# Kernel optimization log

Measured on AMD Instinct MI355X. Metric: run time of the kernel, lower is better.

Reference implementation:

```python
import jax, jax.numpy as jnp
import numpy as np

N = 100000   # nodes
S = 2        # layout samples per graph
G = 8        # graphs in batch
E = 400000   # directed edges
MID = 256    # mid_ch
L = 4        # n_layer
CLN = 2      # concat_last_n
IN_CH = 53 + 32 + 6 * 23 + 6 * 3 + 6 * 4  # 265


def setup_inputs() -> dict:
    key = jax.random.key(0)
    ks = jax.random.split(key, 16)
    f = lambda k, sh: jax.random.normal(k, sh, dtype=jnp.float32)
    return {
        "x_feat": f(ks[0], (N, 53)),
        "dim_feat": f(ks[1], (N, 6, 23)),
        "layout_feat": f(ks[2], (N, S, 6, 4)),
        "tile_feat": f(ks[3], (G, S, 6, 3)),
        "opcode_embed": f(ks[4], (121, 32)) * 0.02,
        "preW": f(ks[5], (IN_CH, MID)) * 0.05,
        "preb": jnp.zeros((MID,), jnp.float32),
        "convWl": f(ks[6], (L, MID, MID // 2)) * 0.05,
        "convWr": f(ks[7], (L, MID, MID // 2)) * 0.05,
        "convb": jnp.zeros((L, MID // 2), jnp.float32),
        "revWl": f(ks[8], (L, MID, MID // 2)) * 0.05,
        "revWr": f(ks[9], (L, MID, MID // 2)) * 0.05,
        "revb": jnp.zeros((L, MID // 2), jnp.float32),
        "headW": f(ks[10], (MID * CLN, 1)) * 0.05,
        "headb": jnp.zeros((1,), jnp.float32),
        "node_opcode": jax.random.randint(ks[11], (N,), 0, 121),
        "batch": jnp.sort(jax.random.randint(ks[12], (N,), 0, G)),
        "edge_index": jax.random.randint(ks[13], (2, E), 0, N),
    }


def _sage(x, src, tgt, inv_deg, Wl, Wr, b):
    # PyG SAGEConv: out = lin_l(mean_{j->i} x_j) + lin_r(x_i) + bias
    # x: [S, N, C]; gather messages from src, scatter-add into tgt.
    agg = jnp.zeros_like(x).at[:, tgt].add(x[:, src])
    agg = agg * inv_deg[None, :, None]
    return (jnp.einsum('snc,co->sno', agg, Wl)
            + jnp.einsum('snc,co->sno', x, Wr) + b)


def reference(x_feat, dim_feat, layout_feat, tile_feat, opcode_embed,
              preW, preb, convWl, convWr, convb, revWl, revWr, revb,
              headW, headb, node_opcode, batch, edge_index):
    op = opcode_embed[node_opcode]                       # [N, 32]
    base = jnp.concatenate([x_feat, op, dim_feat.reshape(N, -1)], axis=-1)
    x = jnp.concatenate([
        jnp.broadcast_to(base[None], (S,) + base.shape),          # [S,N,223]
        layout_feat.transpose(1, 0, 2, 3).reshape(S, N, -1),       # [S,N,24]
        tile_feat[batch].transpose(1, 0, 2, 3).reshape(S, N, -1),  # [S,N,18]
    ], axis=-1)                                                    # [S,N,265]
    x = jax.nn.relu(x @ preW + preb)                               # [S,N,MID]

    src, tgt = edge_index[0], edge_index[1]
    one = jnp.ones((E,), x.dtype)
    inv_fwd = 1.0 / jnp.maximum(jnp.zeros((N,), x.dtype).at[tgt].add(one), 1.0)
    inv_rev = 1.0 / jnp.maximum(jnp.zeros((N,), x.dtype).at[src].add(one), 1.0)

    xs = []
    for i in range(L):
        x = jnp.concatenate([
            _sage(x, src, tgt, inv_fwd, convWl[i], convWr[i], convb[i]),
            _sage(x, tgt, src, inv_rev, revWl[i], revWr[i], revb[i]),
        ], axis=-1)
        x = jax.nn.relu(x)
        if i >= L - CLN:
            xs.append(x)
    x = jnp.concatenate(xs, axis=-1)                     # [S, N, MID*CLN]

    pooled = jnp.zeros((S, G, x.shape[-1]), x.dtype).at[:, batch].add(x)
    out = pooled @ headW + headb                         # [S, G, 1]
    return out.transpose(1, 0, 2)                        # [G, S, 1]
```

## Files before the change

kernel.cpp:

```cpp
#include <hip/hip_runtime.h>
#include <hip/hip_bf16.h>

#define N_NODES 100000
#define S_SAMP 2
#define G_GRAPH 8
#define E_EDGES 400000
#define NLAYER 4
#define IN_CH 265
#define KBASE 256
#define MT128 ((N_NODES + 127) / 128)
#define NPAD (MT128 * 128)
#define NG128 ((MT128 + 7) / 8)
#define NB1 ((N_NODES + 1023) / 1024)

typedef unsigned short u16;
typedef unsigned int u32;
typedef short bf16x8 __attribute__((ext_vector_type(8)));
typedef float f32x4 __attribute__((ext_vector_type(4)));

__device__ __forceinline__ float b2f(u16 u) {
    union { u32 i; float f; } x; x.i = ((u32)u) << 16; return x.f;
}
__device__ __forceinline__ u16 f2b(float f) {
    __hip_bfloat16 h = __float2bfloat16(f);
    return *reinterpret_cast<u16*>(&h);
}

__device__ __forceinline__ void gl_lds16(const u16* g, u16* l) {
    __builtin_amdgcn_global_load_lds(
        (const __attribute__((address_space(1))) void*)g,
        (__attribute__((address_space(3))) void*)l, 16, 0, 0);
}

__global__ __launch_bounds__(256) void build_base_k(const float* __restrict__ xf,
                                                    const float* __restrict__ dimf,
                                                    const float* __restrict__ opemb,
                                                    const int* __restrict__ opcode,
                                                    u16* __restrict__ xb) {
    int item = blockIdx.x * blockDim.x + threadIdx.x;
    int n = item >> 6;
    if (n >= N_NODES) return;
    int base = (item & 63) * 4;
    int opc = opcode[n];
    ushort4 o;
    u16* op = &o.x;
    #pragma unroll
    for (int u = 0; u < 4; u++) {
        int c = base + u;
        float v = 0.0f;
        if (c < 53)       v = xf[(size_t)n * 53 + c];
        else if (c < 85)  v = opemb[opc * 32 + (c - 53)];
        else if (c < 223) v = dimf[(size_t)n * 138 + (c - 85)];
        op[u] = f2b(v);
    }
    *(ushort4*)(xb + (size_t)n * KBASE + base) = o;
}

__global__ void pack_w_k(const float* __restrict__ cWl, const float* __restrict__ rWl,
                         const float* __restrict__ cWr, const float* __restrict__ rWr,
                         const float* __restrict__ cb,  const float* __restrict__ rb,
                         u16* __restrict__ Wt, float* __restrict__ bcat) {
    int idx = blockIdx.x * blockDim.x + threadIdx.x;
    if (idx < NLAYER * 512 * 256) {
        int l = idx >> 17;
        int r = idx & 131071;
        int j = r >> 8;
        int k = r & 255;
        int jj = j & 255;
        int half = j >> 8;
        int sub = jj >> 7;
        int col = jj & 127;
        const float* src = half ? (sub ? rWl : cWl) : (sub ? rWr : cWr);
        Wt[idx] = f2b(src[((size_t)l * 256 + k) * 128 + col]);
    }
    if (idx < NLAYER * 512) {
        int l = idx >> 9;
        int j = idx & 511;
        float v = 0.0f;
        if (j < 256) v = (j < 128) ? cb[l * 128 + j] : rb[l * 128 + (j - 128)];
        bcat[idx] = v;
    }
}

__global__ void pack_pre_k(const float* __restrict__ preW, u16* __restrict__ preWt) {
    int idx = blockIdx.x * blockDim.x + threadIdx.x;
    if (idx >= 256 * KBASE) return;
    int j = idx >> 8;
    int k = idx & 255;
    preWt[idx] = (k < 223) ? f2b(preW[(size_t)k * 256 + j]) : (u16)0;
}

__global__ void tvec_k(const float* __restrict__ tilef, const float* __restrict__ preW,
                       float* __restrict__ tvec) {
    int idx = blockIdx.x * blockDim.x + threadIdx.x;
    if (idx >= G_GRAPH * S_SAMP * 256) return;
    int c = idx & 255;
    int gs = idx >> 8;
    float a = 0.0f;
    #pragma unroll
    for (int k = 0; k < 18; k++)
        a += tilef[gs * 18 + k] * preW[(size_t)(247 + k) * 256 + c];
    tvec[idx] = a;
}

__global__ void deg_k(const int* __restrict__ ei, int* __restrict__ degF,
                      int* __restrict__ degR) {
    int e = blockIdx.x * blockDim.x + threadIdx.x;
    if (e < E_EDGES) {
        atomicAdd(&degF[ei[E_EDGES + e]], 1);
        atomicAdd(&degR[ei[e]], 1);
    }
}

__global__ __launch_bounds__(1024) void scan1_k(const int* __restrict__ degF,
                                                const int* __restrict__ degR,
                                                int* __restrict__ rpF,
                                                int* __restrict__ rpR,
                                                int* __restrict__ bsum) {
    const int* deg = blockIdx.y ? degR : degF;
    int* rp = blockIdx.y ? rpR : rpF;
    __shared__ int buf[1024];
    int i = blockIdx.x * 1024 + threadIdx.x;
    int v = (i < N_NODES) ? deg[i] : 0;
    buf[threadIdx.x] = v;
    __syncthreads();
    for (int off = 1; off < 1024; off <<= 1) {
        int t = (threadIdx.x >= off) ? buf[threadIdx.x - off] : 0;
        __syncthreads();
        buf[threadIdx.x] += t;
        __syncthreads();
    }
    if (i < N_NODES) rp[i] = buf[threadIdx.x] - v;
    if (threadIdx.x == 1023) bsum[blockIdx.y * NB1 + blockIdx.x] = buf[1023];
}

__global__ __launch_bounds__(256) void scan2_k(int* __restrict__ bsum,
                                               int* __restrict__ rpF,
                                               int* __restrict__ rpR) {
    __shared__ int buf[2][128];
    int half = threadIdx.x >> 7;
    int t = threadIdx.x & 127;
    int v = (t < NB1) ? bsum[half * NB1 + t] : 0;
    buf[half][t] = v;
    __syncthreads();
    for (int off = 1; off < 128; off <<= 1) {
        int x = (t >= off) ? buf[half][t - off] : 0;
        __syncthreads();
        buf[half][t] += x;
        __syncthreads();
    }
    if (t < NB1) bsum[half * NB1 + t] = buf[half][t] - v;
    if (t == NB1) (half ? rpR : rpF)[N_NODES] = buf[half][NB1 - 1];
}

__global__ void scan3_k(const int* __restrict__ bsum, int* __restrict__ rpF,
                        int* __restrict__ rpR) {
    int* rp = blockIdx.y ? rpR : rpF;
    int i = blockIdx.x * 1024 + threadIdx.x;
    if (i < N_NODES) rp[i] += bsum[blockIdx.y * NB1 + blockIdx.x];
}

__global__ void inv_cursor_k(const int* __restrict__ degF, const int* __restrict__ degR,
                             const int* __restrict__ rpF, const int* __restrict__ rpR,
                             float* __restrict__ invF, float* __restrict__ invR,
                             int* __restrict__ curF, int* __restrict__ curR) {
    int i = blockIdx.x * blockDim.x + threadIdx.x;
    if (i < N_NODES) {
        invF[i] = 1.0f / fmaxf((float)degF[i], 1.0f);
        invR[i] = 1.0f / fmaxf((float)degR[i], 1.0f);
        curF[i] = rpF[i];
        curR[i] = rpR[i];
    }
}

__global__ void fill_k(const int* __restrict__ ei, int* __restrict__ curF,
                       int* __restrict__ curR, int* __restrict__ colF,
                       int* __restrict__ colR) {
    int e = blockIdx.x * blockDim.x + threadIdx.x;
    if (e < E_EDGES) {
        int s = ei[e], t = ei[E_EDGES + e];
        colF[atomicAdd(&curF[t], 1)] = s;
        colR[atomicAdd(&curR[s], 1)] = t;
    }
}

template <bool RELU_OUT, int NCHUNK, int COLT>
__global__ __launch_bounds__(256) void mmB_k(const u16* __restrict__ A,
                                             const u16* __restrict__ Bt,
                                             const float* __restrict__ bias,
                                             u16* __restrict__ C0,
                                             u16* __restrict__ C1,
                                             int M) {
    __shared__ u16 As[128 * 128];
    __shared__ u16 Bs[64 * 128];
    constexpr int K = NCHUNK * 128;

    int bid = blockIdx.x;
    int x = bid & 7;
    int q = bid >> 3;
    int c = q % COLT;
    int g = q / COLT;
    int rowTile = g * 8 + x;
    if (rowTile >= MT128) return;
    int rowBase = rowTile * 128;
    int colBase = c * 64;

    int tid = threadIdx.x;
    int wv = tid >> 6;
    int lane = tid & 63;
    int quad = lane >> 4;
    int l16 = lane & 15;
    int rsub = lane >> 4;
    int sl = lane & 15;

    f32x4 acc[2][4] = {};

    for (int ci = 0; ci < NCHUNK; ci++) {
        int k0 = ci * 128;
        #pragma unroll
        for (int i = 0; i < 8; i++) {
            int r = wv * 32 + 4 * i + rsub;
            int ch = sl ^ (r & 15);
            gl_lds16(A + (size_t)(rowBase + r) * K + k0 + ch * 8,
                     As + (wv * 32 + 4 * i) * 128);
        }
        #pragma unroll
        for (int i = 0; i < 4; i++) {
            int r = wv * 16 + 4 * i + rsub;
            int ch = sl ^ (r & 15);
            gl_lds16(Bt + (size_t)(colBase + r) * K + k0 + ch * 8,
                     Bs + (wv * 16 + 4 * i) * 128);
        }
        __syncthreads();
        #pragma unroll
        for (int ks = 0; ks < 4; ks++) {
            int ca = ks * 4 + quad;
            bf16x8 af[2];
            #pragma unroll
            for (int rf = 0; rf < 2; rf++) {
                int ra = wv * 32 + rf * 16 + l16;
                af[rf] = *(const bf16x8*)(As + ra * 128 + (ca ^ (ra & 15)) * 8);
            }
            #pragma unroll
            for (int cf = 0; cf < 4; cf++) {
                int rb = cf * 16 + l16;
                bf16x8 bf = *(const bf16x8*)(Bs + rb * 128 + (ca ^ (rb & 15)) * 8);
                acc[0][cf] = __builtin_amdgcn_mfma_f32_16x16x32_bf16(af[0], bf, acc[0][cf], 0, 0, 0);
                acc[1][cf] = __builtin_amdgcn_mfma_f32_16x16x32_bf16(af[1], bf, acc[1][cf], 0, 0, 0);
            }
        }
        if (ci + 1 < NCHUNK) __syncthreads();
    }

    u16* dst = (colBase < 256) ? C0 : C1;
    int cb = colBase & 255;
    #pragma unroll
    for (int rf = 0; rf < 2; rf++) {
        #pragma unroll
        for (int cf = 0; cf < 4; cf++) {
            int col = cb + cf * 16 + l16;
            float bv = bias[colBase + cf * 16 + l16];
            #pragma unroll
            for (int r = 0; r < 4; r++) {
                int row = rowBase + wv * 32 + rf * 16 + quad * 4 + r;
                if (row < M) {
                    float v = acc[rf][cf][r] + bv;
                    if (RELU_OUT) v = fmaxf(v, 0.0f);
                    dst[(size_t)row * 256 + col] = f2b(v);
                }
            }
        }
    }
}

__global__ __launch_bounds__(256) void pre_fix_k(const u16* __restrict__ Xmid,
                                                 const float* __restrict__ layf,
                                                 const float* __restrict__ preW,
                                                 const float* __restrict__ tvec,
                                                 const int* __restrict__ batch,
                                                 int s, u16* __restrict__ X0) {
    __shared__ float tv[G_GRAPH * 256];
    for (int i = threadIdx.x; i < G_GRAPH * 256; i += 256) {
        int g = i >> 8, c = i & 255;
        tv[i] = tvec[(g * S_SAMP + s) * 256 + c];
    }
    __syncthreads();

    int wv = threadIdx.x >> 6;
    int lane = threadIdx.x & 63;
    int c0 = lane * 4;

    float4 W[24];
    #pragma unroll
    for (int k = 0; k < 24; k++)
        W[k] = *(const float4*)(preW + (size_t)(223 + k) * 256 + c0);

    for (int n = blockIdx.x * 4 + wv; n < N_NODES; n += gridDim.x * 4) {
        int g = batch[n];
        float4 L4[6];
        const float4* lp = (const float4*)(layf + ((size_t)n * S_SAMP + s) * 24);
        #pragma unroll
        for (int q = 0; q < 6; q++) L4[q] = lp[q];
        const float* l = (const float*)L4;
        float4 t4 = *(const float4*)&tv[g * 256 + c0];
        float a0 = t4.x, a1 = t4.y, a2 = t4.z, a3 = t4.w;
        #pragma unroll
        for (int k = 0; k < 24; k++) {
            float lk = l[k];
            a0 += lk * W[k].x;
            a1 += lk * W[k].y;
            a2 += lk * W[k].z;
            a3 += lk * W[k].w;
        }
        ushort4 m = *(const ushort4*)(Xmid + (size_t)n * 256 + c0);
        ushort4 o;
        o.x = f2b(fmaxf(b2f(m.x) + a0, 0.0f));
        o.y = f2b(fmaxf(b2f(m.y) + a1, 0.0f));
        o.z = f2b(fmaxf(b2f(m.z) + a2, 0.0f));
        o.w = f2b(fmaxf(b2f(m.w) + a3, 0.0f));
        *(ushort4*)(X0 + (size_t)n * 256 + c0) = o;
    }
}

template <bool DOT>
__global__ __launch_bounds__(256) void agg_k(const int* __restrict__ rpF,
                                             const int* __restrict__ colF,
                                             const int* __restrict__ rpR,
                                             const int* __restrict__ colR,
                                             const float* __restrict__ invF,
                                             const float* __restrict__ invR,
                                             const u16* __restrict__ H,
                                             u16* __restrict__ Xn,
                                             const float* __restrict__ w,
                                             float* __restrict__ dotbuf) {
    int n = (blockIdx.x * blockDim.x + threadIdx.x) >> 6;
    if (n >= N_NODES) return;
    int lane = threadIdx.x & 63;
    int half = lane >> 5;
    int l32 = lane & 31;
    const int* rp  = half ? rpR : rpF;
    const int* col = half ? colR : colF;
    float inv = half ? invR[n] : invF[n];
    const u16* Hb = H + half * 128 + 4 * l32;

    float a0 = 0, a1 = 0, a2 = 0, a3 = 0;
    int b = rp[n], e = rp[n + 1];
    int j = b;
    for (; j + 7 < e; j += 8) {
        int c0 = col[j],     c1 = col[j + 1], c2 = col[j + 2], c3 = col[j + 3];
        int c4 = col[j + 4], c5 = col[j + 5], c6 = col[j + 6], c7 = col[j + 7];
        ushort4 h0 = *(const ushort4*)(Hb + (size_t)c0 * 256);
        ushort4 h1 = *(const ushort4*)(Hb + (size_t)c1 * 256);
        ushort4 h2 = *(const ushort4*)(Hb + (size_t)c2 * 256);
        ushort4 h3 = *(const ushort4*)(Hb + (size_t)c3 * 256);
        ushort4 h4 = *(const ushort4*)(Hb + (size_t)c4 * 256);
        ushort4 h5 = *(const ushort4*)(Hb + (size_t)c5 * 256);
        ushort4 h6 = *(const ushort4*)(Hb + (size_t)c6 * 256);
        ushort4 h7 = *(const ushort4*)(Hb + (size_t)c7 * 256);
        a0 += b2f(h0.x) + b2f(h1.x) + b2f(h2.x) + b2f(h3.x)
            + b2f(h4.x) + b2f(h5.x) + b2f(h6.x) + b2f(h7.x);
        a1 += b2f(h0.y) + b2f(h1.y) + b2f(h2.y) + b2f(h3.y)
            + b2f(h4.y) + b2f(h5.y) + b2f(h6.y) + b2f(h7.y);
        a2 += b2f(h0.z) + b2f(h1.z) + b2f(h2.z) + b2f(h3.z)
            + b2f(h4.z) + b2f(h5.z) + b2f(h6.z) + b2f(h7.z);
        a3 += b2f(h0.w) + b2f(h1.w) + b2f(h2.w) + b2f(h3.w)
            + b2f(h4.w) + b2f(h5.w) + b2f(h6.w) + b2f(h7.w);
    }
    for (; j + 3 < e; j += 4) {
        int c0 = col[j], c1 = col[j + 1], c2 = col[j + 2], c3 = col[j + 3];
        ushort4 h0 = *(const ushort4*)(Hb + (size_t)c0 * 256);
        ushort4 h1 = *(const ushort4*)(Hb + (size_t)c1 * 256);
        ushort4 h2 = *(const ushort4*)(Hb + (size_t)c2 * 256);
        ushort4 h3 = *(const ushort4*)(Hb + (size_t)c3 * 256);
        a0 += b2f(h0.x) + b2f(h1.x) + b2f(h2.x) + b2f(h3.x);
        a1 += b2f(h0.y) + b2f(h1.y) + b2f(h2.y) + b2f(h3.y);
        a2 += b2f(h0.z) + b2f(h1.z) + b2f(h2.z) + b2f(h3.z);
        a3 += b2f(h0.w) + b2f(h1.w) + b2f(h2.w) + b2f(h3.w);
    }
    for (; j < e; j++) {
        int c = col[j];
        ushort4 h = *(const ushort4*)(Hb + (size_t)c * 256);
        a0 += b2f(h.x); a1 += b2f(h.y); a2 += b2f(h.z); a3 += b2f(h.w);
    }
    u16* xp = Xn + (size_t)n * 256 + 4 * lane;
    ushort4 xv = *(const ushort4*)xp;
    float v0 = fmaxf(b2f(xv.x) + a0 * inv, 0.0f);
    float v1 = fmaxf(b2f(xv.y) + a1 * inv, 0.0f);
    float v2 = fmaxf(b2f(xv.z) + a2 * inv, 0.0f);
    float v3 = fmaxf(b2f(xv.w) + a3 * inv, 0.0f);
    ushort4 o;
    o.x = f2b(v0); o.y = f2b(v1); o.z = f2b(v2); o.w = f2b(v3);
    *(ushort4*)xp = o;
    if (DOT) {
        float4 wv4 = *(const float4*)(w + 4 * lane);
        float d = v0 * wv4.x + v1 * wv4.y + v2 * wv4.z + v3 * wv4.w;
        #pragma unroll
        for (int off = 32; off > 0; off >>= 1) d += __shfl_down(d, off);
        if (lane == 0) dotbuf[n] = d;
    }
}

__global__ void out_init_k(float* __restrict__ out, const float* __restrict__ headb) {
    int i = threadIdx.x;
    if (i < G_GRAPH * S_SAMP) out[i] = headb[0];
}

__global__ __launch_bounds__(256) void reduce_k(const float* __restrict__ dotbuf,
                                                const int* __restrict__ batch,
                                                float* __restrict__ out, int s) {
    __shared__ float part[G_GRAPH];
    if (threadIdx.x < G_GRAPH) part[threadIdx.x] = 0.0f;
    __syncthreads();
    for (int i = blockIdx.x * 256 + threadIdx.x; i < N_NODES; i += gridDim.x * 256)
        atomicAdd(&part[batch[i]], dotbuf[i]);
    __syncthreads();
    if (threadIdx.x < G_GRAPH)
        atomicAdd(&out[threadIdx.x * S_SAMP + s], part[threadIdx.x]);
}

extern "C" void kernel_launch(void* const* d_in, const int* in_sizes, int n_in,
                              void* d_out, int out_size, void* d_ws, size_t ws_size,
                              hipStream_t stream) {
    const float* x_feat      = (const float*)d_in[0];
    const float* dim_feat    = (const float*)d_in[1];
    const float* layout_feat = (const float*)d_in[2];
    const float* tile_feat   = (const float*)d_in[3];
    const float* opemb       = (const float*)d_in[4];
    const float* preW        = (const float*)d_in[5];
    const float* preb        = (const float*)d_in[6];
    const float* convWl      = (const float*)d_in[7];
    const float* convWr      = (const float*)d_in[8];
    const float* convb       = (const float*)d_in[9];
    const float* revWl       = (const float*)d_in[10];
    const float* revWr       = (const float*)d_in[11];
    const float* revb        = (const float*)d_in[12];
    const float* headW       = (const float*)d_in[13];
    const float* headb       = (const float*)d_in[14];
    const int*   node_opcode = (const int*)d_in[15];
    const int*   batch       = (const int*)d_in[16];
    const int*   edge_index  = (const int*)d_in[17];
    float* out = (float*)d_out;

    char* ws = (char*)d_ws;
    size_t off = 0;
    auto alloc = [&](size_t nbytes) {
        char* p = ws + off;
        off += (nbytes + 255) & ~(size_t)255;
        return p;
    };
    u16* XA    = (u16*)alloc((size_t)NPAD * 256 * 2);
    u16* XB    = (u16*)alloc((size_t)NPAD * 256 * 2);
    u16* XbH   = (u16*)alloc((size_t)NPAD * 256 * 2);
    u16* Xmid  = (u16*)alloc((size_t)NPAD * 256 * 2);
    u16* Wt    = (u16*)alloc((size_t)NLAYER * 512 * 256 * 2);
    u16* preWt = (u16*)alloc((size_t)256 * KBASE * 2);
    float* bcat   = (float*)alloc(NLAYER * 512 * 4);
    float* tvec   = (float*)alloc(G_GRAPH * S_SAMP * 256 * 4);
    float* dotbuf = (float*)alloc((size_t)N_NODES * 4);
    int* degF  = (int*)alloc(N_NODES * 4);
    int* degR  = (int*)alloc(N_NODES * 4);
    int* rpF   = (int*)alloc((N_NODES + 1) * 4);
    int* rpR   = (int*)alloc((N_NODES + 1) * 4);
    int* curF  = (int*)alloc(N_NODES * 4);
    int* curR  = (int*)alloc(N_NODES * 4);
    int* colF  = (int*)alloc(E_EDGES * 4);
    int* colR  = (int*)alloc(E_EDGES * 4);
    int* bsum  = (int*)alloc(2 * NB1 * 4);
    float* invF = (float*)alloc(N_NODES * 4);
    float* invR = (float*)alloc(N_NODES * 4);

    hipMemsetAsync(degF, 0, N_NODES * 4, stream);
    hipMemsetAsync(degR, 0, N_NODES * 4, stream);

    pack_w_k<<<(NLAYER * 512 * 256 + 255) / 256, 256, 0, stream>>>(
        convWl, revWl, convWr, revWr, convb, revb, Wt, bcat);
    pack_pre_k<<<(256 * KBASE + 255) / 256, 256, 0, stream>>>(preW, preWt);
    tvec_k<<<(G_GRAPH * S_SAMP * 256 + 255) / 256, 256, 0, stream>>>(
        tile_feat, preW, tvec);
    deg_k<<<(E_EDGES + 255) / 256, 256, 0, stream>>>(edge_index, degF, degR);
    scan1_k<<<dim3(NB1, 2), 1024, 0, stream>>>(degF, degR, rpF, rpR, bsum);
    scan2_k<<<1, 256, 0, stream>>>(bsum, rpF, rpR);
    scan3_k<<<dim3(NB1, 2), 1024, 0, stream>>>(bsum, rpF, rpR);
    inv_cursor_k<<<(N_NODES + 255) / 256, 256, 0, stream>>>(
        degF, degR, rpF, rpR, invF, invR, curF, curR);
    fill_k<<<(E_EDGES + 255) / 256, 256, 0, stream>>>(edge_index, curF, curR, colF, colR);
    out_init_k<<<1, 64, 0, stream>>>(out, headb);

    build_base_k<<<(N_NODES * 64 + 255) / 256, 256, 0, stream>>>(
        x_feat, dim_feat, opemb, node_opcode, XbH);
    mmB_k<false, 2, 4><<<NG128 * 8 * 4, 256, 0, stream>>>(
        XbH, preWt, preb, Xmid, Xmid, N_NODES);

    const int gridL   = NG128 * 8 * 8;
    const int gridAgg = (N_NODES * 64 + 255) / 256;

    for (int s = 0; s < S_SAMP; s++) {
        pre_fix_k<<<2048, 256, 0, stream>>>(
            Xmid, layout_feat, preW, tvec, batch, s, XA);

        u16* ins[NLAYER]  = {XA, XB, XA, XB};
        u16* outs[NLAYER] = {XB, XA, XB, XA};
        for (int l = 0; l < NLAYER; l++) {
            mmB_k<false, 2, 8><<<gridL, 256, 0, stream>>>(
                ins[l], Wt + (size_t)l * 512 * 256, bcat + (size_t)l * 512,
                outs[l], XbH, N_NODES);
            if (l < 2) {
                agg_k<false><<<gridAgg, 256, 0, stream>>>(
                    rpF, colF, rpR, colR, invF, invR, XbH, outs[l],
                    nullptr, nullptr);
            } else {
                agg_k<true><<<gridAgg, 256, 0, stream>>>(
                    rpF, colF, rpR, colR, invF, invR, XbH, outs[l],
                    headW + (l == 2 ? 0 : 256), dotbuf);
                reduce_k<<<128, 256, 0, stream>>>(dotbuf, batch, out, s);
            }
        }
    }
}
```

Measured before the change: 1.365 ms.

## Batch both layout samples into single GEMM and aggregation launches

When the workspace is large enough, both samples are processed together: activations are stored as two stacked padded blocks, and each layer issues one GEMM, one aggregation and one reduce over twice the rows instead of looping per sample. This halves the number of launches and gives each kernel more work to fill the GPU. The aggregation kernel also issues the residual and weight loads before the neighbor loop so their latency overlaps the gathers. The cost is roughly double the activation workspace, plus a fallback path that keeps the per-sample loop.

```diff
diff --git a/kernel.cpp b/kernel.cpp
--- a/kernel.cpp
+++ b/kernel.cpp
@@ -10,7 +10,6 @@
 #define KBASE 256
 #define MT128 ((N_NODES + 127) / 128)
 #define NPAD (MT128 * 128)
-#define NG128 ((MT128 + 7) / 8)
 #define NB1 ((N_NODES + 1023) / 1024)
 
 typedef unsigned short u16;
@@ -190,7 +189,7 @@
                                              const float* __restrict__ bias,
                                              u16* __restrict__ C0,
                                              u16* __restrict__ C1,
-                                             int M) {
+                                             int M, int nRT) {
     __shared__ u16 As[128 * 128];
     __shared__ u16 Bs[64 * 128];
     constexpr int K = NCHUNK * 128;
@@ -201,7 +200,7 @@
     int c = q % COLT;
     int g = q / COLT;
     int rowTile = g * 8 + x;
-    if (rowTile >= MT128) return;
+    if (rowTile >= nRT) return;
     int rowBase = rowTile * 128;
     int colBase = c * 64;
 
@@ -278,12 +277,11 @@
                                                  const float* __restrict__ preW,
                                                  const float* __restrict__ tvec,
                                                  const int* __restrict__ batch,
-                                                 int s, u16* __restrict__ X0) {
-    __shared__ float tv[G_GRAPH * 256];
-    for (int i = threadIdx.x; i < G_GRAPH * 256; i += 256) {
-        int g = i >> 8, c = i & 255;
-        tv[i] = tvec[(g * S_SAMP + s) * 256 + c];
-    }
+                                                 int sBase, int count,
+                                                 u16* __restrict__ X0) {
+    __shared__ float tv[G_GRAPH * S_SAMP * 256];
+    for (int i = threadIdx.x; i < G_GRAPH * S_SAMP * 256; i += 256)
+        tv[i] = tvec[i];
     __syncthreads();
 
     int wv = threadIdx.x >> 6;
@@ -295,14 +293,18 @@
     for (int k = 0; k < 24; k++)
         W[k] = *(const float4*)(preW + (size_t)(223 + k) * 256 + c0);
 
-    for (int n = blockIdx.x * 4 + wv; n < N_NODES; n += gridDim.x * 4) {
+    for (int i = blockIdx.x * 4 + wv; i < count; i += gridDim.x * 4) {
+        int s_local = (i >= N_NODES) ? 1 : 0;
+        int n = i - s_local * N_NODES;
+        int s = sBase + s_local;
+        size_t row = (size_t)s_local * NPAD + n;
         int g = batch[n];
         float4 L4[6];
         const float4* lp = (const float4*)(layf + ((size_t)n * S_SAMP + s) * 24);
         #pragma unroll
         for (int q = 0; q < 6; q++) L4[q] = lp[q];
         const float* l = (const float*)L4;
-        float4 t4 = *(const float4*)&tv[g * 256 + c0];
+        float4 t4 = *(const float4*)&tv[(g * S_SAMP + s) * 256 + c0];
         float a0 = t4.x, a1 = t4.y, a2 = t4.z, a3 = t4.w;
         #pragma unroll
         for (int k = 0; k < 24; k++) {
@@ -318,7 +320,7 @@
         o.y = f2b(fmaxf(b2f(m.y) + a1, 0.0f));
         o.z = f2b(fmaxf(b2f(m.z) + a2, 0.0f));
         o.w = f2b(fmaxf(b2f(m.w) + a3, 0.0f));
-        *(ushort4*)(X0 + (size_t)n * 256 + c0) = o;
+        *(ushort4*)(X0 + row * 256 + c0) = o;
     }
 }
 
@@ -332,16 +334,24 @@
                                              const u16* __restrict__ H,
                                              u16* __restrict__ Xn,
                                              const float* __restrict__ w,
-                                             float* __restrict__ dotbuf) {
-    int n = (blockIdx.x * blockDim.x + threadIdx.x) >> 6;
-    if (n >= N_NODES) return;
+                                             float* __restrict__ dotbuf,
+                                             int count) {
+    int i = (blockIdx.x * blockDim.x + threadIdx.x) >> 6;
+    if (i >= count) return;
+    int s_local = (i >= N_NODES) ? 1 : 0;
+    int n = i - s_local * N_NODES;
+    size_t row = (size_t)s_local * NPAD + n;
     int lane = threadIdx.x & 63;
     int half = lane >> 5;
     int l32 = lane & 31;
     const int* rp  = half ? rpR : rpF;
     const int* col = half ? colR : colF;
     float inv = half ? invR[n] : invF[n];
-    const u16* Hb = H + half * 128 + 4 * l32;
+    const u16* Hb = H + (size_t)s_local * NPAD * 256 + half * 128 + 4 * l32;
+
+    u16* xp = Xn + row * 256 + 4 * lane;
+    ushort4 xv = *(const ushort4*)xp;
+    float4 wv4 = DOT ? *(const float4*)(w + 4 * lane) : float4{0, 0, 0, 0};
 
     float a0 = 0, a1 = 0, a2 = 0, a3 = 0;
     int b = rp[n], e = rp[n + 1];
@@ -382,8 +392,6 @@
         ushort4 h = *(const ushort4*)(Hb + (size_t)c * 256);
         a0 += b2f(h.x); a1 += b2f(h.y); a2 += b2f(h.z); a3 += b2f(h.w);
     }
-    u16* xp = Xn + (size_t)n * 256 + 4 * lane;
-    ushort4 xv = *(const ushort4*)xp;
     float v0 = fmaxf(b2f(xv.x) + a0 * inv, 0.0f);
     float v1 = fmaxf(b2f(xv.y) + a1 * inv, 0.0f);
     float v2 = fmaxf(b2f(xv.z) + a2 * inv, 0.0f);
@@ -392,11 +400,10 @@
     o.x = f2b(v0); o.y = f2b(v1); o.z = f2b(v2); o.w = f2b(v3);
     *(ushort4*)xp = o;
     if (DOT) {
-        float4 wv4 = *(const float4*)(w + 4 * lane);
         float d = v0 * wv4.x + v1 * wv4.y + v2 * wv4.z + v3 * wv4.w;
         #pragma unroll
         for (int off = 32; off > 0; off >>= 1) d += __shfl_down(d, off);
-        if (lane == 0) dotbuf[n] = d;
+        if (lane == 0) dotbuf[i] = d;
     }
 }
 
@@ -407,15 +414,19 @@
 
 __global__ __launch_bounds__(256) void reduce_k(const float* __restrict__ dotbuf,
                                                 const int* __restrict__ batch,
-                                                float* __restrict__ out, int s) {
-    __shared__ float part[G_GRAPH];
-    if (threadIdx.x < G_GRAPH) part[threadIdx.x] = 0.0f;
+                                                float* __restrict__ out,
+                                                int sBase, int count) {
+    __shared__ float part[G_GRAPH * S_SAMP];
+    if (threadIdx.x < G_GRAPH * S_SAMP) part[threadIdx.x] = 0.0f;
     __syncthreads();
-    for (int i = blockIdx.x * 256 + threadIdx.x; i < N_NODES; i += gridDim.x * 256)
-        atomicAdd(&part[batch[i]], dotbuf[i]);
+    for (int i = blockIdx.x * 256 + threadIdx.x; i < count; i += gridDim.x * 256) {
+        int s_local = (i >= N_NODES) ? 1 : 0;
+        int n = i - s_local * N_NODES;
+        atomicAdd(&part[batch[n] * S_SAMP + sBase + s_local], dotbuf[i]);
+    }
     __syncthreads();
-    if (threadIdx.x < G_GRAPH)
-        atomicAdd(&out[threadIdx.x * S_SAMP + s], part[threadIdx.x]);
+    if (threadIdx.x < G_GRAPH * S_SAMP)
+        atomicAdd(&out[threadIdx.x], part[threadIdx.x]);
 }
 
 extern "C" void kernel_launch(void* const* d_in, const int* in_sizes, int n_in,
@@ -441,6 +452,10 @@
     const int*   edge_index  = (const int*)d_in[17];
     float* out = (float*)d_out;
 
+    const size_t xrow_bytes2 = (size_t)2 * NPAD * 256 * 2;
+    const bool batched = ws_size >= 3 * xrow_bytes2 + ((size_t)16 << 20);
+    const int NS = batched ? 2 : 1;
+
     char* ws = (char*)d_ws;
     size_t off = 0;
     auto alloc = [&](size_t nbytes) {
@@ -448,15 +463,18 @@
         off += (nbytes + 255) & ~(size_t)255;
         return p;
     };
-    u16* XA    = (u16*)alloc((size_t)NPAD * 256 * 2);
-    u16* XB    = (u16*)alloc((size_t)NPAD * 256 * 2);
-    u16* XbH   = (u16*)alloc((size_t)NPAD * 256 * 2);
-    u16* Xmid  = (u16*)alloc((size_t)NPAD * 256 * 2);
+    const size_t xrows = (size_t)NS * NPAD;
+    u16* XA = (u16*)alloc(xrows * 256 * 2);
+    u16* XB = (u16*)alloc(xrows * 256 * 2);
+    u16* H  = (u16*)alloc(xrows * 256 * 2);
+    u16* base = H;
+    u16* Xmid = batched ? H + (size_t)NPAD * 256
+                        : (u16*)alloc((size_t)NPAD * 256 * 2);
     u16* Wt    = (u16*)alloc((size_t)NLAYER * 512 * 256 * 2);
     u16* preWt = (u16*)alloc((size_t)256 * KBASE * 2);
     float* bcat   = (float*)alloc(NLAYER * 512 * 4);
     float* tvec   = (float*)alloc(G_GRAPH * S_SAMP * 256 * 4);
-    float* dotbuf = (float*)alloc((size_t)N_NODES * 4);
+    float* dotbuf = (float*)alloc((size_t)NS * N_NODES * 4);
     int* degF  = (int*)alloc(N_NODES * 4);
     int* degR  = (int*)alloc(N_NODES * 4);
     int* rpF   = (int*)alloc((N_NODES + 1) * 4);
@@ -487,33 +505,60 @@
     out_init_k<<<1, 64, 0, stream>>>(out, headb);
 
     build_base_k<<<(N_NODES * 64 + 255) / 256, 256, 0, stream>>>(
-        x_feat, dim_feat, opemb, node_opcode, XbH);
-    mmB_k<false, 2, 4><<<NG128 * 8 * 4, 256, 0, stream>>>(
-        XbH, preWt, preb, Xmid, Xmid, N_NODES);
-
-    const int gridL   = NG128 * 8 * 8;
-    const int gridAgg = (N_NODES * 64 + 255) / 256;
-
-    for (int s = 0; s < S_SAMP; s++) {
-        pre_fix_k<<<2048, 256, 0, stream>>>(
-            Xmid, layout_feat, preW, tvec, batch, s, XA);
+        x_feat, dim_feat, opemb, node_opcode, base);
+    mmB_k<false, 2, 4><<<((MT128 + 7) / 8) * 8 * 4, 256, 0, stream>>>(
+        base, preWt, preb, Xmid, Xmid, N_NODES, MT128);
+
+    if (batched) {
+        const int count = 2 * N_NODES;
+        const int nRT = 2 * MT128;
+        const int gridL = ((nRT + 7) / 8) * 8 * 8;
+        const int gridAgg = (count * 64 + 255) / 256;
+        const int Mv = NPAD + N_NODES;
+
+        pre_fix_k<<<4096, 256, 0, stream>>>(
+            Xmid, layout_feat, preW, tvec, batch, 0, count, XA);
 
         u16* ins[NLAYER]  = {XA, XB, XA, XB};
         u16* outs[NLAYER] = {XB, XA, XB, XA};
         for (int l = 0; l < NLAYER; l++) {
             mmB_k<false, 2, 8><<<gridL, 256, 0, stream>>>(
                 ins[l], Wt + (size_t)l * 512 * 256, bcat + (size_t)l * 512,
-                outs[l], XbH, N_NODES);
+                outs[l], H, Mv, nRT);
             if (l < 2) {
                 agg_k<false><<<gridAgg, 256, 0, stream>>>(
-                    rpF, colF, rpR, colR, invF, invR, XbH, outs[l],
-                    nullptr, nullptr);
+                    rpF, colF, rpR, colR, invF, invR, H, outs[l],
+                    nullptr, nullptr, count);
             } else {
                 agg_k<true><<<gridAgg, 256, 0, stream>>>(
-                    rpF, colF, rpR, colR, invF, invR, XbH, outs[l],
-                    headW + (l == 2 ? 0 : 256), dotbuf);
-                reduce_k<<<128, 256, 0, stream>>>(dotbuf, batch, out, s);
+                    rpF, colF, rpR, colR, invF, invR, H, outs[l],
+                    headW + (l == 2 ? 0 : 256), dotbuf, count);
+                reduce_k<<<128, 256, 0, stream>>>(dotbuf, batch, out, 0, count);
             }
         }
-    }
-}
+    } else {
+        const int gridL = ((MT128 + 7) / 8) * 8 * 8;
+        const int gridAgg = (N_NODES * 64 + 255) / 256;
+        for (int s = 0; s < S_SAMP; s++) {
+            pre_fix_k<<<2048, 256, 0, stream>>>(
+                Xmid, layout_feat, preW, tvec, batch, s, N_NODES, XA);
+            u16* ins[NLAYER]  = {XA, XB, XA, XB};
+            u16* outs[NLAYER] = {XB, XA, XB, XA};
+            for (int l = 0; l < NLAYER; l++) {
+                mmB_k<false, 2, 8><<<gridL, 256, 0, stream>>>(
+                    ins[l], Wt + (size_t)l * 512 * 256, bcat + (size_t)l * 512,
+                    outs[l], H, N_NODES, MT128);
+                if (l < 2) {
+                    agg_k<false><<<gridAgg, 256, 0, stream>>>(
+                        rpF, colF, rpR, colR, invF, invR, H, outs[l],
+                        nullptr, nullptr, N_NODES);
+                } else {
+                    agg_k<true><<<gridAgg, 256, 0, stream>>>(
+                        rpF, colF, rpR, colR, invF, invR, H, outs[l],
+                        headW + (l == 2 ? 0 : 256), dotbuf, N_NODES);
+                    reduce_k<<<128, 256, 0, stream>>>(dotbuf, batch, out, s, N_NODES);
+                }
+            }
+        }
+    }
+}
```

New measurement: 1.366 ms. No clear change (+0.1%).
